# Performance work log

Measured on AMD Instinct MI355X. Metric: run time of the kernel, lower is better.

The kernel has to match this reference:

```python
import jax, jax.numpy as jnp
from jax import lax
import numpy as np

B = 262144
CLASSES = 11


def setup_inputs() -> dict:
    key = jax.random.key(0)
    ks = jax.random.split(key, 8)
    exponents = jax.random.randint(ks[0], (B, 16), 0, CLASSES, dtype=jnp.int32)
    conv0_w = jax.random.normal(ks[1], (4, 12, 1, 2), jnp.float32) * 0.1
    conv0_b = jax.random.normal(ks[2], (4,), jnp.float32) * 0.05
    conv1_w = jax.random.normal(ks[3], (4, 12, 2, 1), jnp.float32) * 0.1
    # xavier-uniform linears, bias filled with 0.01 (as in init_weights)
    lim1 = float(np.sqrt(6.0 / (96 + 256)))
    linear_w = jax.random.uniform(ks[4], (256, 96), jnp.float32, -lim1, lim1)
    linear_b = jnp.full((256,), 0.01, jnp.float32)
    lim2 = float(np.sqrt(6.0 / (256 + 4)))
    out_w = jax.random.uniform(ks[5], (4, 256), jnp.float32, -lim2, lim2)
    out_b = jnp.full((4,), 0.01, jnp.float32)
    return {"exponents": exponents, "conv0_w": conv0_w, "conv0_b": conv0_b,
            "conv1_w": conv1_w, "linear_w": linear_w, "linear_b": linear_b,
            "out_w": out_w, "out_b": out_b}


def _conv(x, w):
    return lax.conv_general_dilated(x, w, (1, 1), 'VALID',
                                    dimension_numbers=('NCHW', 'OIHW', 'NCHW'))


def _forward(exponents, conv0_w, conv0_b, conv1_w, linear_w, linear_b, out_w, out_b):
    e = exponents.reshape(-1, 4, 4)
    # reconstruct board values: 0 tile stays 0, else 2**e
    x = jnp.where(e == 0, 0.0, jnp.exp2(e.astype(jnp.float32)))  # [B,4,4]
    # rotate_normalize: flips chosen from argmax corner (computed BEFORE flipping)
    corners = jnp.stack([x[:, 0, 0], x[:, 0, -1], x[:, -1, 0], x[:, -1, -1]], axis=1)
    ix = jnp.argmax(corners, axis=1)
    flip_v = ix >= 2          # floor(ix/2) == 1
    flip_h = (ix % 2) == 1
    x = jnp.where(flip_v[:, None, None], x[:, ::-1, :], x)
    x = jnp.where(flip_h[:, None, None], x[:, :, ::-1], x)
    # log2 with 0 -> 0, one-hot over 11 classes
    x_log = jnp.log2(x + (x == 0).astype(jnp.float32))
    onehot = jax.nn.one_hot(jnp.round(x_log).astype(jnp.int32), CLASSES,
                            dtype=jnp.float32)          # [B,4,4,11]
    onehot = jnp.transpose(onehot, (0, 3, 1, 2))         # [B,11,4,4]
    mask = onehot.sum(axis=1, keepdims=True)             # channel 0 (all ones)
    feat = jnp.concatenate([mask, onehot], axis=1)       # [B,12,4,4]
    zh = jax.nn.relu(_conv(feat, conv0_w) + conv0_b[None, :, None, None])  # [B,4,4,3]
    zv = jax.nn.relu(_conv(feat, conv1_w))                                  # [B,4,3,4]
    z1 = jnp.concatenate([zh.reshape(-1, 48), zv.reshape(-1, 48)], axis=1)  # [B,96]
    z2 = jax.nn.relu(z1 @ linear_w.T + linear_b)                            # [B,256]
    probs = jax.nn.softmax(z2 @ out_w.T + out_b, axis=1)                    # [B,4]
    # unscramble: vert swaps actions (0,1); horiz swaps actions (2,3)
    perm = jnp.stack([jnp.where(flip_v, 1, 0), jnp.where(flip_v, 0, 1),
                      jnp.where(flip_h, 3, 2), jnp.where(flip_h, 2, 3)], axis=1)
    return jnp.take_along_axis(probs, perm, axis=1)


def reference(exponents, conv0_w, conv0_b, conv1_w, linear_w, linear_b, out_w, out_b):
    return _forward(exponents, conv0_w, conv0_b, conv1_w, linear_w, linear_b, out_w, out_b)
```

## Files before the change

### kernel.cpp

```cpp
#include <hip/hip_runtime.h>

typedef unsigned int  u32;
typedef unsigned short u16;

typedef float    f4  __attribute__((ext_vector_type(4)));
typedef short    bf8 __attribute__((ext_vector_type(8)));
typedef __fp16   h8  __attribute__((ext_vector_type(8)));
typedef __fp16   h2  __attribute__((ext_vector_type(2)));

#define NBLK  1024
#define ITERS 4
#define ZSTR  104

__device__ __forceinline__ u32 bfr(float f) {
    union { float f; u32 u; } v; v.f = f;
    return (v.u + 0x7fffu + ((v.u >> 16) & 1u)) >> 16;
}
__device__ __forceinline__ u32 pk2(float lo, float hi) { return bfr(lo) | (bfr(hi) << 16); }
__device__ __forceinline__ u32 pkh(float lo, float hi) {
    union { h2 h; u32 u; } v; v.h = __builtin_amdgcn_cvt_pkrtz(lo, hi); return v.u;
}
__device__ __forceinline__ u32 nrev(u32 x) {
    return ((x >> 12) & 0xFu) | ((x >> 4) & 0xF0u) | ((x << 4) & 0xF00u) | ((x << 12) & 0xF000u);
}

__launch_bounds__(256, 4)
__global__ void smartcnn_fused(const int* __restrict__ exps,
                               const float* __restrict__ c0w, const float* __restrict__ c0b,
                               const float* __restrict__ c1w,
                               const float* __restrict__ lw,  const float* __restrict__ lb,
                               const float* __restrict__ ow,  const float* __restrict__ ob,
                               float* __restrict__ out)
{
    __shared__ uint2  ThA[121];
    __shared__ uint2  TvA[121];
    __shared__ u16    z1[64 * ZSTR];
    __shared__ float4 Pbuf[4][4][16];
    __shared__ u32    flg[64];

    const int tid  = threadIdx.x;
    const int w    = tid >> 6;
    const int lane = tid & 63;
    const int m    = lane & 15;
    const int qd   = lane >> 4;


    for (int i = tid; i < 121; i += 256) {
        int v1 = i / 11, v2 = i - v1 * 11;
        float hv[4], vv[4];
        #pragma unroll
        for (int c = 0; c < 4; ++c) {
            hv[c] = fmaxf(c0w[c*24 + 0] + c0w[c*24 + (1+v1)*2 + 0] + c0b[c]
                        + c0w[c*24 + 1] + c0w[c*24 + (1+v2)*2 + 1], 0.f);
            vv[c] = fmaxf(c1w[c*24 + 0] + c1w[c*24 + (1+v1)*2 + 0]
                        + c1w[c*24 + 1] + c1w[c*24 + (1+v2)*2 + 1], 0.f);
        }
        ThA[i] = make_uint2(pk2(hv[0], hv[1]), pk2(hv[2], hv[3]));
        TvA[i] = make_uint2(pk2(vv[0], vv[1]), pk2(vv[2], vv[3]));
    }

    bf8 af[4][3];
    {
        u16* srow = &z1[(w*16 + m) * ZSTR];
        #pragma unroll
        for (int tt = 0; tt < 4; ++tt) {
            const int tbase = ((tt & 1) ? 4 : 0) + ((tt >> 1) ? 32 : 0);
            const int fid = 64*w + tbase + 8*(m >> 2) + (m & 3);
            const float* rowp = lw + (size_t)fid*96 + qd*24;
            #pragma unroll
            for (int v = 0; v < 6; ++v) {
                float4 x = *(const float4*)(rowp + v*4);
                u16 e[4] = {(u16)bfr(x.x), (u16)bfr(x.y), (u16)bfr(x.z), (u16)bfr(x.w)};
                #pragma unroll
                for (int j = 0; j < 4; ++j) {
                    int ko = qd*24 + v*4 + j;
                    int kp = (ko < 48) ? ((ko % 12)*4 + ko/12)
                                       : (48 + ((ko - 48) % 12)*4 + (ko - 48)/12);
                    srow[kp] = e[j];
                }
            }
            #pragma unroll
            for (int s = 0; s < 3; ++s)
                af[tt][s] = *(const bf8*)(srow + s*32 + qd*8);
        }
    }
    u32 owA[2][4];
    #pragma unroll
    for (int c = 0; c < 2; ++c) {
        int n8 = 64*w + 32*c + qd*8;
        #pragma unroll
        for (int k = 0; k < 4; ++k)
            owA[c][k] = (m < 4) ? pkh(ow[m*256 + n8 + 2*k], ow[m*256 + n8 + 2*k + 1]) : 0u;
    }
    f4 lb4[4];
    #pragma unroll
    for (int tt = 0; tt < 4; ++tt) {
        const int tbase = ((tt & 1) ? 4 : 0) + ((tt >> 1) ? 32 : 0);
        lb4[tt] = *(const f4*)(lb + 64*w + tbase + 8*qd);
    }
    const float4 obv = *(const float4*)ob;

    const int b0 = blockIdx.x * (ITERS * 64);
    __syncthreads();

    int4 e4 = *(const int4*)(exps + (size_t)(b0 + w*16 + m)*16 + qd*4);
    u32 fl = 0;

    #pragma unroll 1
    for (int it = 0; it < ITERS; ++it) {
        if (it > 0) {
            float4 s0 = Pbuf[qd][0][m], s1 = Pbuf[qd][1][m];
            float4 s2 = Pbuf[qd][2][m], s3 = Pbuf[qd][3][m];
            float L0 = s0.x + s1.x + s2.x + s3.x + obv.x;
            float L1 = s0.y + s1.y + s2.y + s3.y + obv.y;
            float L2 = s0.z + s1.z + s2.z + s3.z + obv.z;
            float L3 = s0.w + s1.w + s2.w + s3.w + obv.w;
            float mx = fmaxf(fmaxf(L0, L1), fmaxf(L2, L3));
            float e0 = __expf(L0 - mx), e1 = __expf(L1 - mx), e2 = __expf(L2 - mx), e3 = __expf(L3 - mx);
            float inv = 1.0f / (e0 + e1 + e2 + e3);
            float p0 = e0 * inv, p1 = e1 * inv, p2 = e2 * inv, p3 = e3 * inv;
            float4 o;
            o.x = (fl & 1u) ? p1 : p0;
            o.y = (fl & 1u) ? p0 : p1;
            o.z = (fl & 2u) ? p3 : p2;
            o.w = (fl & 2u) ? p2 : p3;
            *(float4*)(out + (size_t)(b0 + (it-1)*64 + qd*16 + m) * 4) = o;
        }

        {
            u32 pkd = (u32)e4.x | ((u32)e4.y << 4) | ((u32)e4.z << 8) | ((u32)e4.w << 12);
            u32 R0 = (u32)__shfl((int)pkd, m);
            u32 R1 = (u32)__shfl((int)pkd, m + 16);
            u32 R2 = (u32)__shfl((int)pkd, m + 32);
            u32 R3 = (u32)__shfl((int)pkd, m + 48);
            u32 c0v = R0 & 15u, c1v = (R0 >> 12) & 15u, c2v = R3 & 15u, c3v = (R3 >> 12) & 15u;
            u32 best = c0v; int ix = 0;
            if (c1v > best) { best = c1v; ix = 1; }
            if (c2v > best) { best = c2v; ix = 2; }
            if (c3v > best) { best = c3v; ix = 3; }
            const bool fv = (ix >= 2), fh = ((ix & 1) != 0);
            u32 F[4];
            F[0] = fv ? R3 : R0;
            F[1] = fv ? R2 : R1;
            F[2] = fv ? R1 : R2;
            F[3] = fv ? R0 : R3;
            #pragma unroll
            for (int i = 0; i < 4; ++i) F[i] = fh ? nrev(F[i]) : F[i];

            if (qd == 0) flg[w*16 + m] = (u32)fv | ((u32)fh << 1);

            const u32 Fq = F[qd];
            u32 nbq[4], nbc[4];
            #pragma unroll
            for (int j = 0; j < 4; ++j) nbq[j] = (Fq >> (4*j)) & 15u;
            #pragma unroll
            for (int i = 0; i < 4; ++i) nbc[i] = (F[i] >> (4*qd)) & 15u;

            uint2 H0 = ThA[nbq[0]*11u + nbq[1]];
            uint2 H1 = ThA[nbq[1]*11u + nbq[2]];
            uint2 H2 = ThA[nbq[2]*11u + nbq[3]];
            uint2 V0 = TvA[nbc[0]*11u + nbc[1]];
            uint2 V1 = TvA[nbc[1]*11u + nbc[2]];
            uint2 V2 = TvA[nbc[2]*11u + nbc[3]];

            u16* zrow = &z1[(w*16 + m) * ZSTR];
            *(uint2*)(zrow + (qd*3 + 0)*4) = H0;
            *(uint2*)(zrow + (qd*3 + 1)*4) = H1;
            *(uint2*)(zrow + (qd*3 + 2)*4) = H2;
            *(uint2*)(zrow + 48 + (0*4 + qd)*4) = V0;
            *(uint2*)(zrow + 48 + (1*4 + qd)*4) = V1;
            *(uint2*)(zrow + 48 + (2*4 + qd)*4) = V2;
        }

        if (it + 1 < ITERS)
            e4 = *(const int4*)(exps + (size_t)(b0 + (it+1)*64 + w*16 + m)*16 + qd*4);

        __syncthreads();

        fl = flg[qd*16 + m];

        #pragma unroll
        for (int G = 0; G < 4; ++G) {
            bf8 zb[3];
            #pragma unroll
            for (int s = 0; s < 3; ++s)
                zb[s] = *(const bf8*)(&z1[(G*16 + m)*ZSTR + s*32 + qd*8]);

            f4 acc_t[4] = {lb4[0], lb4[1], lb4[2], lb4[3]};
            #pragma unroll
            for (int s = 0; s < 3; ++s)
                #pragma unroll
                for (int tt = 0; tt < 4; ++tt)
                    acc_t[tt] = __builtin_amdgcn_mfma_f32_16x16x32_bf16(af[tt][s], zb[s], acc_t[tt], 0, 0, 0);

            f4 acc2 = {0.f, 0.f, 0.f, 0.f};
            #pragma unroll
            for (int c = 0; c < 2; ++c) {
                union { u32 u[4]; h8 v; } bu, au;
                bu.u[0] = pkh(fmaxf(acc_t[2*c  ][0], 0.f), fmaxf(acc_t[2*c  ][1], 0.f));
                bu.u[1] = pkh(fmaxf(acc_t[2*c  ][2], 0.f), fmaxf(acc_t[2*c  ][3], 0.f));
                bu.u[2] = pkh(fmaxf(acc_t[2*c+1][0], 0.f), fmaxf(acc_t[2*c+1][1], 0.f));
                bu.u[3] = pkh(fmaxf(acc_t[2*c+1][2], 0.f), fmaxf(acc_t[2*c+1][3], 0.f));
                au.u[0] = owA[c][0]; au.u[1] = owA[c][1]; au.u[2] = owA[c][2]; au.u[3] = owA[c][3];
                acc2 = __builtin_amdgcn_mfma_f32_16x16x32_f16(au.v, bu.v, acc2, 0, 0, 0);
            }
            if (qd == 0)
                Pbuf[G][w][m] = make_float4(acc2[0], acc2[1], acc2[2], acc2[3]);
        }
        __syncthreads();
    }

    {
        float4 s0 = Pbuf[qd][0][m], s1 = Pbuf[qd][1][m];
        float4 s2 = Pbuf[qd][2][m], s3 = Pbuf[qd][3][m];
        float L0 = s0.x + s1.x + s2.x + s3.x + obv.x;
        float L1 = s0.y + s1.y + s2.y + s3.y + obv.y;
        float L2 = s0.z + s1.z + s2.z + s3.z + obv.z;
        float L3 = s0.w + s1.w + s2.w + s3.w + obv.w;
        float mx = fmaxf(fmaxf(L0, L1), fmaxf(L2, L3));
        float e0 = __expf(L0 - mx), e1 = __expf(L1 - mx), e2 = __expf(L2 - mx), e3 = __expf(L3 - mx);
        float inv = 1.0f / (e0 + e1 + e2 + e3);
        float p0 = e0 * inv, p1 = e1 * inv, p2 = e2 * inv, p3 = e3 * inv;
        float4 o;
        o.x = (fl & 1u) ? p1 : p0;
        o.y = (fl & 1u) ? p0 : p1;
        o.z = (fl & 2u) ? p3 : p2;
        o.w = (fl & 2u) ? p2 : p3;
        *(float4*)(out + (size_t)(b0 + (ITERS-1)*64 + qd*16 + m) * 4) = o;
    }
}

extern "C" void kernel_launch(void* const* d_in, const int* in_sizes, int n_in,
                              void* d_out, int out_size, void* d_ws, size_t ws_size,
                              hipStream_t stream) {
    const int*   exps = (const int*)  d_in[0];
    const float* c0w  = (const float*)d_in[1];
    const float* c0b  = (const float*)d_in[2];
    const float* c1w  = (const float*)d_in[3];
    const float* lw   = (const float*)d_in[4];
    const float* lbv  = (const float*)d_in[5];
    const float* oww  = (const float*)d_in[6];
    const float* obv  = (const float*)d_in[7];
    smartcnn_fused<<<NBLK, 256, 0, stream>>>(exps, c0w, c0b, c1w, lw, lbv, oww, obv, (float*)d_out);
}
```

Baseline: 104.0 us.

## Double-buffer z1/Pbuf/flags to overlap feature build with MFMA GEMM

```diff
diff --git a/kernel.cpp b/kernel.cpp
--- a/kernel.cpp
+++ b/kernel.cpp
@@ -22,6 +22,109 @@
 }
 __device__ __forceinline__ u32 nrev(u32 x) {
     return ((x >> 12) & 0xFu) | ((x >> 4) & 0xF0u) | ((x << 4) & 0xF00u) | ((x << 12) & 0xF000u);
+}
+
+__device__ __forceinline__ void phase1_fn(const int4 e4, u16* __restrict__ z1b, u32* __restrict__ flgb,
+                                          const uint2* __restrict__ Th, const uint2* __restrict__ Tv,
+                                          const int w, const int m, const int qd)
+{
+    u32 pkd = (u32)e4.x | ((u32)e4.y << 4) | ((u32)e4.z << 8) | ((u32)e4.w << 12);
+    u32 R0 = (u32)__shfl((int)pkd, m);
+    u32 R1 = (u32)__shfl((int)pkd, m + 16);
+    u32 R2 = (u32)__shfl((int)pkd, m + 32);
+    u32 R3 = (u32)__shfl((int)pkd, m + 48);
+    u32 c0v = R0 & 15u, c1v = (R0 >> 12) & 15u, c2v = R3 & 15u, c3v = (R3 >> 12) & 15u;
+    u32 best = c0v; int ix = 0;
+    if (c1v > best) { best = c1v; ix = 1; }
+    if (c2v > best) { best = c2v; ix = 2; }
+    if (c3v > best) { best = c3v; ix = 3; }
+    const bool fv = (ix >= 2), fh = ((ix & 1) != 0);
+    u32 F[4];
+    F[0] = fv ? R3 : R0;
+    F[1] = fv ? R2 : R1;
+    F[2] = fv ? R1 : R2;
+    F[3] = fv ? R0 : R3;
+    #pragma unroll
+    for (int i = 0; i < 4; ++i) F[i] = fh ? nrev(F[i]) : F[i];
+
+    if (qd == 0) flgb[w*16 + m] = (u32)fv | ((u32)fh << 1);
+
+    const u32 Fq = F[qd];
+    u32 nbq[4], nbc[4];
+    #pragma unroll
+    for (int j = 0; j < 4; ++j) nbq[j] = (Fq >> (4*j)) & 15u;
+    #pragma unroll
+    for (int i = 0; i < 4; ++i) nbc[i] = (F[i] >> (4*qd)) & 15u;
+
+    uint2 H0 = Th[nbq[0]*11u + nbq[1]];
+    uint2 H1 = Th[nbq[1]*11u + nbq[2]];
+    uint2 H2 = Th[nbq[2]*11u + nbq[3]];
+    uint2 V0 = Tv[nbc[0]*11u + nbc[1]];
+    uint2 V1 = Tv[nbc[1]*11u + nbc[2]];
+    uint2 V2 = Tv[nbc[2]*11u + nbc[3]];
+
+    u16* zrow = &z1b[(w*16 + m) * ZSTR];
+    *(uint2*)(zrow + (qd*3 + 0)*4) = H0;
+    *(uint2*)(zrow + (qd*3 + 1)*4) = H1;
+    *(uint2*)(zrow + (qd*3 + 2)*4) = H2;
+    *(uint2*)(zrow + 48 + (0*4 + qd)*4) = V0;
+    *(uint2*)(zrow + 48 + (1*4 + qd)*4) = V1;
+    *(uint2*)(zrow + 48 + (2*4 + qd)*4) = V2;
+}
+
+__device__ __forceinline__ void gemm_fn(const u16* __restrict__ z1b, float4* __restrict__ Pb,
+                                        const bf8 (&af)[4][3], const u32 (&owA)[2][4], const f4 (&lb4)[4],
+                                        const int w, const int m, const int qd)
+{
+    #pragma unroll
+    for (int G = 0; G < 4; ++G) {
+        bf8 zb[3];
+        #pragma unroll
+        for (int s = 0; s < 3; ++s)
+            zb[s] = *(const bf8*)(&z1b[(G*16 + m)*ZSTR + s*32 + qd*8]);
+
+        f4 acc_t[4] = {lb4[0], lb4[1], lb4[2], lb4[3]};
+        #pragma unroll
+        for (int s = 0; s < 3; ++s)
+            #pragma unroll
+            for (int tt = 0; tt < 4; ++tt)
+                acc_t[tt] = __builtin_amdgcn_mfma_f32_16x16x32_bf16(af[tt][s], zb[s], acc_t[tt], 0, 0, 0);
+
+        f4 acc2 = {0.f, 0.f, 0.f, 0.f};
+        #pragma unroll
+        for (int c = 0; c < 2; ++c) {
+            union { u32 u[4]; h8 v; } bu, au;
+            bu.u[0] = pkh(fmaxf(acc_t[2*c  ][0], 0.f), fmaxf(acc_t[2*c  ][1], 0.f));
+            bu.u[1] = pkh(fmaxf(acc_t[2*c  ][2], 0.f), fmaxf(acc_t[2*c  ][3], 0.f));
+            bu.u[2] = pkh(fmaxf(acc_t[2*c+1][0], 0.f), fmaxf(acc_t[2*c+1][1], 0.f));
+            bu.u[3] = pkh(fmaxf(acc_t[2*c+1][2], 0.f), fmaxf(acc_t[2*c+1][3], 0.f));
+            au.u[0] = owA[c][0]; au.u[1] = owA[c][1]; au.u[2] = owA[c][2]; au.u[3] = owA[c][3];
+            acc2 = __builtin_amdgcn_mfma_f32_16x16x32_f16(au.v, bu.v, acc2, 0, 0, 0);
+        }
+        if (qd == 0)
+            Pb[(G*4 + w)*16 + m] = make_float4(acc2[0], acc2[1], acc2[2], acc2[3]);
+    }
+}
+
+__device__ __forceinline__ void epi_fn(const float4* __restrict__ Pb, const u32 fl, const float4 obv,
+                                       float* __restrict__ out, const int base, const int m, const int qd)
+{
+    float4 s0 = Pb[(qd*4 + 0)*16 + m], s1 = Pb[(qd*4 + 1)*16 + m];
+    float4 s2 = Pb[(qd*4 + 2)*16 + m], s3 = Pb[(qd*4 + 3)*16 + m];
+    float L0 = s0.x + s1.x + s2.x + s3.x + obv.x;
+    float L1 = s0.y + s1.y + s2.y + s3.y + obv.y;
+    float L2 = s0.z + s1.z + s2.z + s3.z + obv.z;
+    float L3 = s0.w + s1.w + s2.w + s3.w + obv.w;
+    float mx = fmaxf(fmaxf(L0, L1), fmaxf(L2, L3));
+    float e0 = __expf(L0 - mx), e1 = __expf(L1 - mx), e2 = __expf(L2 - mx), e3 = __expf(L3 - mx);
+    float inv = 1.0f / (e0 + e1 + e2 + e3);
+    float p0 = e0 * inv, p1 = e1 * inv, p2 = e2 * inv, p3 = e3 * inv;
+    float4 o;
+    o.x = (fl & 1u) ? p1 : p0;
+    o.y = (fl & 1u) ? p0 : p1;
+    o.z = (fl & 2u) ? p3 : p2;
+    o.w = (fl & 2u) ? p2 : p3;
+    *(float4*)(out + (size_t)(base + qd*16 + m) * 4) = o;
 }
 
 __launch_bounds__(256, 4)
@@ -34,9 +137,12 @@
 {
     __shared__ uint2  ThA[121];
     __shared__ uint2  TvA[121];
-    __shared__ u16    z1[64 * ZSTR];
-    __shared__ float4 Pbuf[4][4][16];
-    __shared__ u32    flg[64];
+    __shared__ u16    z1A[64 * ZSTR];
+    __shared__ u16    z1B[64 * ZSTR];
+    __shared__ float4 PbA[4*4*16];
+    __shared__ float4 PbB[4*4*16];
+    __shared__ u32    flgA[64];
+    __shared__ u32    flgB[64];
 
     const int tid  = threadIdx.x;
     const int w    = tid >> 6;
@@ -44,7 +150,6 @@
     const int m    = lane & 15;
     const int qd   = lane >> 4;
 
-
     for (int i = tid; i < 121; i += 256) {
         int v1 = i / 11, v2 = i - v1 * 11;
         float hv[4], vv[4];
@@ -61,7 +166,7 @@
 
     bf8 af[4][3];
     {
-        u16* srow = &z1[(w*16 + m) * ZSTR];
+        u16* srow = &z1A[(w*16 + m) * ZSTR];
         #pragma unroll
         for (int tt = 0; tt < 4; ++tt) {
             const int tbase = ((tt & 1) ? 4 : 0) + ((tt >> 1) ? 32 : 0);
@@ -104,129 +209,34 @@
     __syncthreads();
 
     int4 e4 = *(const int4*)(exps + (size_t)(b0 + w*16 + m)*16 + qd*4);
-    u32 fl = 0;
+    phase1_fn(e4, z1A, flgA, &ThA[0], &TvA[0], w, m, qd);
+    e4 = *(const int4*)(exps + (size_t)(b0 + 64 + w*16 + m)*16 + qd*4);
+    __syncthreads();
 
     #pragma unroll 1
-    for (int it = 0; it < ITERS; ++it) {
-        if (it > 0) {
-            float4 s0 = Pbuf[qd][0][m], s1 = Pbuf[qd][1][m];
-            float4 s2 = Pbuf[qd][2][m], s3 = Pbuf[qd][3][m];
-            float L0 = s0.x + s1.x + s2.x + s3.x + obv.x;
-            float L1 = s0.y + s1.y + s2.y + s3.y + obv.y;
-            float L2 = s0.z + s1.z + s2.z + s3.z + obv.z;
-            float L3 = s0.w + s1.w + s2.w + s3.w + obv.w;
-            float mx = fmaxf(fmaxf(L0, L1), fmaxf(L2, L3));
-            float e0 = __expf(L0 - mx), e1 = __expf(L1 - mx), e2 = __expf(L2 - mx), e3 = __expf(L3 - mx);
-            float inv = 1.0f / (e0 + e1 + e2 + e3);
-            float p0 = e0 * inv, p1 = e1 * inv, p2 = e2 * inv, p3 = e3 * inv;
-            float4 o;
-            o.x = (fl & 1u) ? p1 : p0;
-            o.y = (fl & 1u) ? p0 : p1;
-            o.z = (fl & 2u) ? p3 : p2;
-            o.w = (fl & 2u) ? p2 : p3;
-            *(float4*)(out + (size_t)(b0 + (it-1)*64 + qd*16 + m) * 4) = o;
-        }
-
-        {
-            u32 pkd = (u32)e4.x | ((u32)e4.y << 4) | ((u32)e4.z << 8) | ((u32)e4.w << 12);
-            u32 R0 = (u32)__shfl((int)pkd, m);
-            u32 R1 = (u32)__shfl((int)pkd, m + 16);
-            u32 R2 = (u32)__shfl((int)pkd, m + 32);
-            u32 R3 = (u32)__shfl((int)pkd, m + 48);
-            u32 c0v = R0 & 15u, c1v = (R0 >> 12) & 15u, c2v = R3 & 15u, c3v = (R3 >> 12) & 15u;
-            u32 best = c0v; int ix = 0;
-            if (c1v > best) { best = c1v; ix = 1; }
-            if (c2v > best) { best = c2v; ix = 2; }
-            if (c3v > best) { best = c3v; ix = 3; }
-            const bool fv = (ix >= 2), fh = ((ix & 1) != 0);
-            u32 F[4];
-            F[0] = fv ? R3 : R0;
-            F[1] = fv ? R2 : R1;
-            F[2] = fv ? R1 : R2;
-            F[3] = fv ? R0 : R3;
-            #pragma unroll
-            for (int i = 0; i < 4; ++i) F[i] = fh ? nrev(F[i]) : F[i];
-
-            if (qd == 0) flg[w*16 + m] = (u32)fv | ((u32)fh << 1);
-
-            const u32 Fq = F[qd];
-            u32 nbq[4], nbc[4];
-            #pragma unroll
-            for (int j = 0; j < 4; ++j) nbq[j] = (Fq >> (4*j)) & 15u;
-            #pragma unroll
-            for (int i = 0; i < 4; ++i) nbc[i] = (F[i] >> (4*qd)) & 15u;
-
-            uint2 H0 = ThA[nbq[0]*11u + nbq[1]];
-            uint2 H1 = ThA[nbq[1]*11u + nbq[2]];
-            uint2 H2 = ThA[nbq[2]*11u + nbq[3]];
-            uint2 V0 = TvA[nbc[0]*11u + nbc[1]];
-            uint2 V1 = TvA[nbc[1]*11u + nbc[2]];
-            uint2 V2 = TvA[nbc[2]*11u + nbc[3]];
-
-            u16* zrow = &z1[(w*16 + m) * ZSTR];
-            *(uint2*)(zrow + (qd*3 + 0)*4) = H0;
-            *(uint2*)(zrow + (qd*3 + 1)*4) = H1;
-            *(uint2*)(zrow + (qd*3 + 2)*4) = H2;
-            *(uint2*)(zrow + 48 + (0*4 + qd)*4) = V0;
-            *(uint2*)(zrow + 48 + (1*4 + qd)*4) = V1;
-            *(uint2*)(zrow + 48 + (2*4 + qd)*4) = V2;
-        }
-
-        if (it + 1 < ITERS)
-            e4 = *(const int4*)(exps + (size_t)(b0 + (it+1)*64 + w*16 + m)*16 + qd*4);
+    for (int itp = 0; itp < ITERS/2; ++itp) {
+        const int it = itp * 2;
+
+        const u32 flA = flgA[qd*16 + m];
+        phase1_fn(e4, z1B, flgB, &ThA[0], &TvA[0], w, m, qd);
+        if (it + 2 < ITERS)
+            e4 = *(const int4*)(exps + (size_t)(b0 + (it+2)*64 + w*16 + m)*16 + qd*4);
+        gemm_fn(z1A, PbA, af, owA, lb4, w, m, qd);
 
         __syncthreads();
 
-        fl = flg[qd*16 + m];
-
-        #pragma unroll
-        for (int G = 0; G < 4; ++G) {
-            bf8 zb[3];
-            #pragma unroll
-            for (int s = 0; s < 3; ++s)
-                zb[s] = *(const bf8*)(&z1[(G*16 + m)*ZSTR + s*32 + qd*8]);
-
-            f4 acc_t[4] = {lb4[0], lb4[1], lb4[2], lb4[3]};
-            #pragma unroll
-            for (int s = 0; s < 3; ++s)
-                #pragma unroll
-                for (int tt = 0; tt < 4; ++tt)
-                    acc_t[tt] = __builtin_amdgcn_mfma_f32_16x16x32_bf16(af[tt][s], zb[s], acc_t[tt], 0, 0, 0);
-
-            f4 acc2 = {0.f, 0.f, 0.f, 0.f};
-            #pragma unroll
-            for (int c = 0; c < 2; ++c) {
-                union { u32 u[4]; h8 v; } bu, au;
-                bu.u[0] = pkh(fmaxf(acc_t[2*c  ][0], 0.f), fmaxf(acc_t[2*c  ][1], 0.f));
-                bu.u[1] = pkh(fmaxf(acc_t[2*c  ][2], 0.f), fmaxf(acc_t[2*c  ][3], 0.f));
-                bu.u[2] = pkh(fmaxf(acc_t[2*c+1][0], 0.f), fmaxf(acc_t[2*c+1][1], 0.f));
-                bu.u[3] = pkh(fmaxf(acc_t[2*c+1][2], 0.f), fmaxf(acc_t[2*c+1][3], 0.f));
-                au.u[0] = owA[c][0]; au.u[1] = owA[c][1]; au.u[2] = owA[c][2]; au.u[3] = owA[c][3];
-                acc2 = __builtin_amdgcn_mfma_f32_16x16x32_f16(au.v, bu.v, acc2, 0, 0, 0);
-            }
-            if (qd == 0)
-                Pbuf[G][w][m] = make_float4(acc2[0], acc2[1], acc2[2], acc2[3]);
-        }
+        epi_fn(PbA, flA, obv, out, b0 + it*64, m, qd);
+        const u32 flB = flgB[qd*16 + m];
+        if (it + 2 < ITERS) {
+            phase1_fn(e4, z1A, flgA, &ThA[0], &TvA[0], w, m, qd);
+            if (it + 3 < ITERS)
+                e4 = *(const int4*)(exps + (size_t)(b0 + (it+3)*64 + w*16 + m)*16 + qd*4);
+        }
+        gemm_fn(z1B, PbB, af, owA, lb4, w, m, qd);
+
         __syncthreads();
-    }
-
-    {
-        float4 s0 = Pbuf[qd][0][m], s1 = Pbuf[qd][1][m];
-        float4 s2 = Pbuf[qd][2][m], s3 = Pbuf[qd][3][m];
-        float L0 = s0.x + s1.x + s2.x + s3.x + obv.x;
-        float L1 = s0.y + s1.y + s2.y + s3.y + obv.y;
-        float L2 = s0.z + s1.z + s2.z + s3.z + obv.z;
-        float L3 = s0.w + s1.w + s2.w + s3.w + obv.w;
-        float mx = fmaxf(fmaxf(L0, L1), fmaxf(L2, L3));
-        float e0 = __expf(L0 - mx), e1 = __expf(L1 - mx), e2 = __expf(L2 - mx), e3 = __expf(L3 - mx);
-        float inv = 1.0f / (e0 + e1 + e2 + e3);
-        float p0 = e0 * inv, p1 = e1 * inv, p2 = e2 * inv, p3 = e3 * inv;
-        float4 o;
-        o.x = (fl & 1u) ? p1 : p0;
-        o.y = (fl & 1u) ? p0 : p1;
-        o.z = (fl & 2u) ? p3 : p2;
-        o.w = (fl & 2u) ? p2 : p3;
-        *(float4*)(out + (size_t)(b0 + (ITERS-1)*64 + qd*16 + m) * 4) = o;
+
+        epi_fn(PbB, flB, obv, out, b0 + (it+1)*64, m, qd);
     }
 }
 
```

Result: no change. 102.1 us (-1.8%).
